# Kernel tuning notes

Hardware: AMD Instinct MI355X
Metric: run time of the kernel (lower is better)

## Reference

```python
import jax, jax.numpy as jnp
import numpy as np

B, T, C, H = 2, 2048, 1024, 16
HS = C // H                      # head_size = 64
LAYER_IDX = 2
LAMBDA_INIT = 0.8 - 0.6 * float(np.exp(-0.3 * (LAYER_IDX - 1)))
EPS = 1e-12


def setup_inputs() -> dict:
    key = jax.random.key(0)
    ks = jax.random.split(key, 22)
    std = 0.02
    w = lambda k, shape: (jax.random.normal(k, shape, jnp.float32) * std)
    inp = {
        'q': jax.random.normal(ks[0], (B, T, C), jnp.float32),
        'k': jax.random.normal(ks[1], (B, T, C), jnp.float32),
        'v': jax.random.normal(ks[2], (B, T, C), jnp.float32),
        'mask': jax.random.randint(ks[3], (B, T), 0, 2).astype(jnp.int32),
        # projection weights stored as (in, out) so y = x @ W + b
        'Wq1': w(ks[4], (C, C)), 'bq1': jnp.zeros((C,), jnp.float32),
        'Wq2': w(ks[5], (C, C)), 'bq2': jnp.zeros((C,), jnp.float32),
        'Wk1': w(ks[6], (C, C)), 'bk1': jnp.zeros((C,), jnp.float32),
        'Wk2': w(ks[7], (C, C)), 'bk2': jnp.zeros((C,), jnp.float32),
        'Wv':  w(ks[8], (C, 2 * C)), 'bv': jnp.zeros((2 * C,), jnp.float32),
        'Wc':  w(ks[9], (2 * C, C)), 'bc': jnp.zeros((C,), jnp.float32),
        'ln_w': jnp.ones((2 * HS,), jnp.float32),
        'ln_b': jnp.zeros((2 * HS,), jnp.float32),
        'lq1': jax.random.normal(ks[10], (H, HS), jnp.float32) * 0.1,
        'lk1': jax.random.normal(ks[11], (H, HS), jnp.float32) * 0.1,
        'lq2': jax.random.normal(ks[12], (H, HS), jnp.float32) * 0.1,
        'lk2': jax.random.normal(ks[13], (H, HS), jnp.float32) * 0.1,
    }
    return inp


def reference(q, k, v, mask, Wq1, bq1, Wq2, bq2, Wk1, bk1, Wk2, bk2,
              Wv, bv, Wc, bc, ln_w, ln_b, lq1, lk1, lq2, lk2):
    def heads(x, d):  # [B,T,H*d] -> [B,H,T,d]
        return x.reshape(B, T, H, d).transpose(0, 2, 1, 3)

    q1 = heads(q @ Wq1 + bq1, HS)
    q2 = heads(q @ Wq2 + bq2, HS)
    k1 = heads(k @ Wk1 + bk1, HS)
    k2 = heads(k @ Wk2 + bk2, HS)
    vv = heads(v @ Wv + bv, 2 * HS)          # [B,H,T,2*HS]

    scale = 1.0 / np.sqrt(HS)
    att1 = jnp.einsum('bhqd,bhkd->bhqk', q1, k1) * scale
    att2 = jnp.einsum('bhqd,bhkd->bhqk', q2, k2) * scale

    m = (mask == 0)[:, None, :, None]         # [B,1,Tq,1] -> masks query rows
    att1 = jnp.where(m, -1e9, att1)
    att2 = jnp.where(m, -1e9, att2)
    att1 = jax.nn.softmax(att1, axis=-1)
    att2 = jax.nn.softmax(att2, axis=-1)

    lam1 = jnp.exp(jnp.sum(lq1 * lk1, axis=-1))   # [H]
    lam2 = jnp.exp(jnp.sum(lq2 * lk2, axis=-1))
    lam = (lam1 - lam2 + LAMBDA_INIT)[None, :, None, None]
    att = att1 - lam * att2                       # differential attention

    y = jnp.einsum('bhqk,bhkd->bhqd', att, vv)    # [B,H,T,2*HS]

    # per-head TF-style LayerNorm over 2*HS, then (1 - lambda_init) scale
    u = y.mean(-1, keepdims=True)
    s = ((y - u) ** 2).mean(-1, keepdims=True)
    y = ln_w * ((y - u) / jnp.sqrt(s + EPS)) + ln_b
    y = y * (1.0 - LAMBDA_INIT)

    y = y.transpose(0, 2, 1, 3).reshape(B, T, 2 * C)
    return y @ Wc + bc
```

## Files before the change

### kernel.cpp

```cpp
#include <hip/hip_runtime.h>
#include <hip/hip_bf16.h>
#include <stdint.h>


#define T_SEQ 2048

typedef unsigned short u16;
typedef __attribute__((ext_vector_type(8))) short short8;
typedef __attribute__((ext_vector_type(4))) float f32x4;
typedef __attribute__((ext_vector_type(16))) float f32x16;

#define LAMBDA_INIT 0.35550906759096926f
#define ONE_MINUS_LI 0.6444909324090307f
#define SM_SCALE 0.125f
#define LOG2E 1.44269504f

__device__ __forceinline__ u16 f2bf(float f) {
  uint32_t u = __float_as_uint(f);
  return (u16)((u + 0x7FFFu + ((u >> 16) & 1u)) >> 16);
}
__device__ __forceinline__ float b2f(u16 u) {
  return __uint_as_float(((uint32_t)u) << 16);
}
__device__ __forceinline__ short8 ld8(const u16* p) {
  return *reinterpret_cast<const short8*>(p);
}
__device__ __forceinline__ void st8(u16* p, short8 v) {
  *reinterpret_cast<short8*>(p) = v;
}
__device__ __forceinline__ f32x4 mfma16(short8 a, short8 b, f32x4 c) {
  return __builtin_amdgcn_mfma_f32_16x16x32_bf16(a, b, c, 0, 0, 0);
}
__device__ __forceinline__ f32x16 mfma32(short8 a, short8 b, f32x16 c) {
  return __builtin_amdgcn_mfma_f32_32x32x16_bf16(a, b, c, 0, 0, 0);
}
__device__ __forceinline__ uint32_t cvtpk(float lo, float hi_) {
  uint32_t r;
  asm("v_cvt_pk_bf16_f32 %0, %1, %2" : "=v"(r) : "v"(lo), "v"(hi_));
  return r;
}

__global__ __launch_bounds__(256) void cvt_bf16(const float* __restrict__ in,
                                                u16* __restrict__ out, int n) {
  int i = (blockIdx.x * 256 + threadIdx.x) * 4;
  if (i >= n) return;
  float4 f = *reinterpret_cast<const float4*>(in + i);
  union { u16 u[4]; uint2 v; } pk;
  pk.u[0] = f2bf(f.x); pk.u[1] = f2bf(f.y); pk.u[2] = f2bf(f.z); pk.u[3] = f2bf(f.w);
  *reinterpret_cast<uint2*>(out + i) = pk.v;
}

__global__ __launch_bounds__(256) void tcvt(const float* __restrict__ W,
                                            u16* __restrict__ WT,
                                            int K, int N, int outRowOff) {
  __shared__ float tile[32][33];
  int n0 = blockIdx.x * 32, k0 = blockIdx.y * 32;
  int tx = threadIdx.x & 31, ty = threadIdx.x >> 5;
#pragma unroll
  for (int p = 0; p < 4; ++p)
    tile[ty + 8 * p][tx] = W[(size_t)(k0 + ty + 8 * p) * N + n0 + tx];
  __syncthreads();
#pragma unroll
  for (int p = 0; p < 4; ++p)
    WT[(size_t)(outRowOff + n0 + ty + 8 * p) * K + k0 + tx] = f2bf(tile[tx][ty + 8 * p]);
}

__global__ __launch_bounds__(256) void bias_concat(const float* __restrict__ b1,
                                                   const float* __restrict__ b2,
                                                   float* __restrict__ out) {
  int i = blockIdx.x * 256 + threadIdx.x;
  out[i] = (i < 1024) ? b1[i] : b2[i - 1024];
}

#define BM 128
#define BN 128
#define BK 64

template <int EPI, bool QK>
__global__ __launch_bounds__(256) void gemm_bt(const u16* __restrict__ A,
                                               const u16* __restrict__ BT,
                                               const float* __restrict__ bias,
                                               void* __restrict__ Cv,
                                               int M, int N, int K) {
  __shared__ __align__(16) u16 As[BM * BK];
  __shared__ __align__(16) u16 Bs[BN * BK];
  int t = threadIdx.x;
  int w = t >> 6, l = t & 63;
  int g = l >> 4, c16 = l & 15;
  int wr = w >> 1, wc = w & 1;
  size_t gm = (size_t)blockIdx.y * BM, gn = (size_t)blockIdx.x * BN;
  if (QK && gm >= 4096) {
    BT += (size_t)2048 * 1024;
    bias += 2048;
  }

  f32x4 acc[4][4] = {};

  int srow = l >> 3;
  int scol = (l & 7) * 8;
  const u16* Ag = A + (gm + w * 32 + srow) * (size_t)K + scol;
  const u16* Bg = BT + (gn + w * 32 + srow) * (size_t)K + scol;

  for (int kt = 0; kt < K; kt += BK) {
    __syncthreads();
#pragma unroll
    for (int c = 0; c < 4; ++c) {
      __builtin_amdgcn_global_load_lds(
          (const __attribute__((address_space(1))) void*)(Ag + (size_t)(c * 8) * K + kt),
          (__attribute__((address_space(3))) void*)&As[(w * 32 + c * 8) * BK], 16, 0, 0);
      __builtin_amdgcn_global_load_lds(
          (const __attribute__((address_space(1))) void*)(Bg + (size_t)(c * 8) * K + kt),
          (__attribute__((address_space(3))) void*)&Bs[(w * 32 + c * 8) * BK], 16, 0, 0);
    }
    __syncthreads();
#pragma unroll
    for (int kk = 0; kk < 2; ++kk) {
      short8 af[4], bf[4];
#pragma unroll
      for (int m = 0; m < 4; ++m)
        af[m] = *reinterpret_cast<const short8*>(
            &As[(wr * 64 + m * 16 + c16) * BK + kk * 32 + g * 8]);
#pragma unroll
      for (int n = 0; n < 4; ++n)
        bf[n] = *reinterpret_cast<const short8*>(
            &Bs[(wc * 64 + n * 16 + c16) * BK + kk * 32 + g * 8]);
#pragma unroll
      for (int m = 0; m < 4; ++m)
#pragma unroll
        for (int n = 0; n < 4; ++n)
          acc[m][n] = mfma16(af[m], bf[n], acc[m][n]);
    }
  }

#pragma unroll
  for (int m = 0; m < 4; ++m)
#pragma unroll
    for (int n = 0; n < 4; ++n) {
      int row0 = (int)gm + wr * 64 + m * 16 + g * 4;
      int col = (int)gn + wc * 64 + n * 16 + c16;
      float bz = bias[col];
      if (EPI == 0) {
        u16* C = (u16*)Cv;
#pragma unroll
        for (int r = 0; r < 4; ++r)
          C[(size_t)(row0 + r) * N + col] = f2bf(acc[m][n][r] + bz);
      } else if (EPI == 1) {
        u16* C = (u16*)Cv;
        int bb = row0 >> 11, tt = row0 & 2047;
        union { u16 u[4]; uint2 v; } pk;
#pragma unroll
        for (int r = 0; r < 4; ++r) pk.u[r] = f2bf(acc[m][n][r] + bz);
        *reinterpret_cast<uint2*>(&C[((size_t)(bb * 2048 + col)) * 2048 + tt]) = pk.v;
      } else {
        float* C = (float*)Cv;
#pragma unroll
        for (int r = 0; r < 4; ++r)
          C[(size_t)(row0 + r) * N + col] = acc[m][n][r] + bz;
      }
    }
}

#define KROW 72
#define YROW 72
__global__ __launch_bounds__(256, 3) void diffattn(
    const u16* __restrict__ q1q2, const u16* __restrict__ k1k2,
    const u16* __restrict__ vvT, const int* __restrict__ mask,
    const float* __restrict__ lq1, const float* __restrict__ lk1,
    const float* __restrict__ lq2, const float* __restrict__ lk2,
    const float* __restrict__ lnw, const float* __restrict__ lnb,
    u16* __restrict__ yout) {
  __shared__ __align__(16) u16 smem[18432];
  u16* Ksm = smem;
  u16* Vsm = smem + 9216;
  u16* Ysm = smem;

  int tid = threadIdx.x;
  int w = tid >> 6, l = tid & 63;
  int q = l & 31, hi = l >> 5;
  int pair = w >> 1, stream = w & 1;

  int id = blockIdx.x;
  int j = id & 7, rest = id >> 3;
  int xblk = rest & 31, ygrp = rest >> 5;
  int bh = ygrp * 8 + j;
  int b = bh >> 4, h = bh & 15;
  int qr0 = xblk * 64 + pair * 32;

  float lm1 = lq1[h * 64 + l] * lk1[h * 64 + l];
  float lm2 = lq2[h * 64 + l] * lk2[h * 64 + l];
#pragma unroll
  for (int o = 32; o; o >>= 1) {
    lm1 += __shfl_xor(lm1, o);
    lm2 += __shfl_xor(lm2, o);
  }
  float lam = __expf(lm1) - __expf(lm2) + LAMBDA_INIT;

  int soff = stream * 1024;
  const u16* qrow = q1q2 + (size_t)(b * T_SEQ + qr0 + q) * 2048 + h * 64 + soff + hi * 8;
  short8 qf[4];
#pragma unroll
  for (int c = 0; c < 4; ++c) qf[c] = ld8(qrow + c * 16);

  float scale = (mask[b * T_SEQ + qr0 + q] == 0) ? 0.f : (SM_SCALE * LOG2E);

  float M = -INFINITY, L = 0.f;
  f32x16 acc[4] = {};

  int srw = tid >> 1, shalf = tid & 1;
  int kstream = srw >> 6, kkey = srw & 63;
  const u16* srcK =
      k1k2 + (size_t)(b * T_SEQ + kkey) * 2048 + h * 64 + kstream * 1024 + shalf * 32;
  u16* dstK = &Ksm[srw * KROW + shalf * 32];
  const u16* srcV = vvT + ((size_t)(b * 16 + h) * 128 + srw) * 2048 + shalf * 32;
  u16* dstV = &Vsm[srw * KROW + shalf * 32];

  short8 kpre[4], vpre[4];
#pragma unroll
  for (int u = 0; u < 4; ++u) {
    kpre[u] = ld8(srcK + u * 8);
    vpre[u] = ld8(srcV + u * 8);
  }

  for (int kt = 0; kt < T_SEQ; kt += 64) {
    __syncthreads();
#pragma unroll
    for (int u = 0; u < 4; ++u) {
      st8(dstK + u * 8, kpre[u]);
      st8(dstV + u * 8, vpre[u]);
    }
    __syncthreads();
    if (kt + 64 < T_SEQ) {
      const u16* nk = srcK + (size_t)(kt + 64) * 2048;
      const u16* nv = srcV + (kt + 64);
#pragma unroll
      for (int u = 0; u < 4; ++u) {
        kpre[u] = ld8(nk + u * 8);
        vpre[u] = ld8(nv + u * 8);
      }
    }

#pragma unroll
    for (int st = 0; st < 2; ++st) {
      const u16* kbase = &Ksm[(stream * 64 + st * 32 + q) * KROW + hi * 8];
      short8 kf[4];
#pragma unroll
      for (int c = 0; c < 4; ++c) kf[c] = ld8(kbase + c * 16);

      f32x16 s = {};
#pragma unroll
      for (int c = 0; c < 4; ++c) s = mfma32(kf[c], qf[c], s);

      float m0 = fmaxf(fmaxf(s[0], s[1]), s[2]);
      float m1 = fmaxf(fmaxf(s[3], s[4]), s[5]);
      float m2 = fmaxf(fmaxf(s[6], s[7]), s[8]);
      float m3 = fmaxf(fmaxf(s[9], s[10]), s[11]);
      float m4 = fmaxf(fmaxf(s[12], s[13]), s[14]);
      float ma = fmaxf(fmaxf(m0, m1), m2);
      float mb = fmaxf(fmaxf(m3, m4), s[15]);
      float rm = fmaxf(ma, mb);
      rm = fmaxf(rm, __shfl_xor(rm, 32));
      float tm = rm * scale;

      if (!__all(tm - M <= 11.5f)) {
        float Mn = fmaxf(M, tm);
        float a = exp2f(M - Mn);
        L *= a;
#pragma unroll
        for (int d = 0; d < 4; ++d) acc[d] *= a;
        M = Mn;
      }

      float p[16];
#pragma unroll
      for (int r = 0; r < 16; ++r) p[r] = exp2f(__builtin_fmaf(s[r], scale, -M));
      float s8[8], s4[4];
#pragma unroll
      for (int i = 0; i < 8; ++i) s8[i] = p[i] + p[i + 8];
#pragma unroll
      for (int i = 0; i < 4; ++i) s4[i] = s8[i] + s8[i + 4];
      float ps = (s4[0] + s4[1]) + (s4[2] + s4[3]);
      ps += __shfl_xor(ps, 32);
      L += ps;

      uint32_t a1 = cvtpk(p[0], p[1]), a2 = cvtpk(p[2], p[3]);
      uint32_t b1 = cvtpk(p[4], p[5]), b2 = cvtpk(p[6], p[7]);
      uint32_t c1 = cvtpk(p[8], p[9]), c2 = cvtpk(p[10], p[11]);
      uint32_t d1 = cvtpk(p[12], p[13]), d2 = cvtpk(p[14], p[15]);
      uint32_t sa1 = (uint32_t)__shfl_xor((int)a1, 32), sa2 = (uint32_t)__shfl_xor((int)a2, 32);
      uint32_t sb1 = (uint32_t)__shfl_xor((int)b1, 32), sb2 = (uint32_t)__shfl_xor((int)b2, 32);
      uint32_t sc1 = (uint32_t)__shfl_xor((int)c1, 32), sc2 = (uint32_t)__shfl_xor((int)c2, 32);
      uint32_t sd1 = (uint32_t)__shfl_xor((int)d1, 32), sd2 = (uint32_t)__shfl_xor((int)d2, 32);
      union { uint32_t u[4]; short8 s8v; } pu0, pu1;
      pu0.u[0] = hi ? sb1 : a1;  pu0.u[1] = hi ? sb2 : a2;
      pu0.u[2] = hi ? b1 : sa1;  pu0.u[3] = hi ? b2 : sa2;
      pu1.u[0] = hi ? sd1 : c1;  pu1.u[1] = hi ? sd2 : c2;
      pu1.u[2] = hi ? d1 : sc1;  pu1.u[3] = hi ? d2 : sc2;
      short8 pf0 = pu0.s8v, pf1 = pu1.s8v;

#pragma unroll
      for (int d = 0; d < 4; ++d) {
        const u16* vb0 = &Vsm[(d * 32 + q) * KROW + st * 32 + hi * 8];
        short8 vf0 = ld8(vb0);
        short8 vf1 = ld8(vb0 + 16);
        acc[d] = mfma32(vf0, pf0, acc[d]);
        acc[d] = mfma32(vf1, pf1, acc[d]);
      }
    }
  }

  float inv = 1.f / L;
  __syncthreads();
  if (stream == 1) {
    u16* yrow = &Ysm[(pair * 64 + l) * YROW];
#pragma unroll
    for (int d = 0; d < 4; ++d) {
      union { uint32_t u[8]; short8 v[2]; } pk;
#pragma unroll
      for (int i = 0; i < 8; ++i)
        pk.u[i] = cvtpk(acc[d][2 * i] * inv, acc[d][2 * i + 1] * inv);
      st8(yrow + d * 16, pk.v[0]);
      st8(yrow + d * 16 + 8, pk.v[1]);
    }
  }
  __syncthreads();
  if (stream == 0) {
    const u16* yrow = &Ysm[(pair * 64 + l) * YROW];
    float y[4][16];
#pragma unroll
    for (int d = 0; d < 4; ++d) {
      short8 y2a = ld8(yrow + d * 16);
      short8 y2b = ld8(yrow + d * 16 + 8);
#pragma unroll
      for (int i = 0; i < 8; ++i) {
        y[d][i] = acc[d][i] * inv - lam * b2f((u16)y2a[i]);
        y[d][8 + i] = acc[d][8 + i] * inv - lam * b2f((u16)y2b[i]);
      }
    }
    float sm = 0.f;
#pragma unroll
    for (int d = 0; d < 4; ++d)
#pragma unroll
      for (int r = 0; r < 16; ++r) sm += y[d][r];
    sm += __shfl_xor(sm, 32);
    float u = sm * (1.f / 128.f);
    float var = 0.f;
#pragma unroll
    for (int d = 0; d < 4; ++d)
#pragma unroll
      for (int r = 0; r < 16; ++r) { float dd = y[d][r] - u; var += dd * dd; }
    var += __shfl_xor(var, 32);
    float rstd = rsqrtf(var * (1.f / 128.f) + 1e-12f);

    size_t orow = (size_t)(b * T_SEQ + qr0 + q) * 2048 + h * 128;
#pragma unroll
    for (int d = 0; d < 4; ++d)
#pragma unroll
      for (int rr = 0; rr < 4; ++rr) {
        int base = d * 32 + 8 * rr + 4 * hi;
        union { u16 u[4]; uint2 v; } o;
#pragma unroll
        for (int i = 0; i < 4; ++i) {
          float yv = (lnw[base + i] * ((y[d][rr * 4 + i] - u) * rstd) + lnb[base + i]) *
                     ONE_MINUS_LI;
          o.u[i] = f2bf(yv);
        }
        *reinterpret_cast<uint2*>(&yout[orow + base]) = o.v;
      }
  }
}

extern "C" void kernel_launch(void* const* d_in, const int* in_sizes, int n_in,
                              void* d_out, int out_size, void* d_ws, size_t ws_size,
                              hipStream_t stream) {
  (void)in_sizes; (void)n_in; (void)out_size; (void)ws_size;
  const float* q   = (const float*)d_in[0];
  const float* k   = (const float*)d_in[1];
  const float* v   = (const float*)d_in[2];
  const int* maskp = (const int*)d_in[3];
  const float* Wq1 = (const float*)d_in[4];
  const float* bq1 = (const float*)d_in[5];
  const float* Wq2 = (const float*)d_in[6];
  const float* bq2 = (const float*)d_in[7];
  const float* Wk1 = (const float*)d_in[8];
  const float* bk1 = (const float*)d_in[9];
  const float* Wk2 = (const float*)d_in[10];
  const float* bk2 = (const float*)d_in[11];
  const float* Wv  = (const float*)d_in[12];
  const float* bv  = (const float*)d_in[13];
  const float* Wc  = (const float*)d_in[14];
  const float* bc  = (const float*)d_in[15];
  const float* lnw = (const float*)d_in[16];
  const float* lnb = (const float*)d_in[17];
  const float* lq1 = (const float*)d_in[18];
  const float* lk1 = (const float*)d_in[19];
  const float* lq2 = (const float*)d_in[20];
  const float* lk2 = (const float*)d_in[21];

  char* ws = (char*)d_ws;
  u16* qb     = (u16*)(ws + 0);
  u16* kb     = (u16*)(ws + 8388608);
  u16* vb     = (u16*)(ws + 16777216);
  u16* Wq12T  = (u16*)(ws + 25165824);
  u16* Wk12T  = (u16*)(ws + 29360128);
  u16* WvT    = (u16*)(ws + 33554432);
  u16* WcT    = (u16*)(ws + 37748736);
  float* biasq = (float*)(ws + 41943040);
  float* biask = (float*)(ws + 41951232);
  u16* q1q2   = (u16*)(ws + 41959424);
  u16* k1k2   = (u16*)(ws + 58736640);
  u16* vvT    = (u16*)(ws + 75513856);
  u16* yb     = (u16*)(ws + 0);

  const int NELEM = 2 * T_SEQ * 1024;

  cvt_bf16<<<4096, 256, 0, stream>>>(q, qb, NELEM);
  cvt_bf16<<<4096, 256, 0, stream>>>(k, kb, NELEM);
  cvt_bf16<<<4096, 256, 0, stream>>>(v, vb, NELEM);

  tcvt<<<dim3(32, 32), 256, 0, stream>>>(Wq1, Wq12T, 1024, 1024, 0);
  tcvt<<<dim3(32, 32), 256, 0, stream>>>(Wq2, Wq12T, 1024, 1024, 1024);
  tcvt<<<dim3(32, 32), 256, 0, stream>>>(Wk1, Wk12T, 1024, 1024, 0);
  tcvt<<<dim3(32, 32), 256, 0, stream>>>(Wk2, Wk12T, 1024, 1024, 1024);
  tcvt<<<dim3(64, 32), 256, 0, stream>>>(Wv, WvT, 1024, 2048, 0);
  tcvt<<<dim3(32, 64), 256, 0, stream>>>(Wc, WcT, 2048, 1024, 0);

  bias_concat<<<8, 256, 0, stream>>>(bq1, bq2, biasq);
  bias_concat<<<8, 256, 0, stream>>>(bk1, bk2, biask);

  gemm_bt<0, true><<<dim3(16, 64), 256, 0, stream>>>(qb, Wq12T, biasq, q1q2,
                                                     8192, 2048, 1024);
  gemm_bt<1, false><<<dim3(16, 32), 256, 0, stream>>>(vb, WvT, bv, vvT, 4096, 2048, 1024);

  diffattn<<<1024, 256, 0, stream>>>(q1q2, k1k2, vvT, maskp,
                                     lq1, lk1, lq2, lk2, lnw, lnb, yb);

  gemm_bt<2, false><<<dim3(8, 32), 256, 0, stream>>>(yb, WcT, bc, d_out, 4096, 1024, 2048);
}
```

Before: 327.7 us.

## Use head-contiguous K layout and larger 512-thread attention blocks

```diff
diff --git a/kernel.cpp b/kernel.cpp
--- a/kernel.cpp
+++ b/kernel.cpp
@@ -139,31 +139,41 @@
       int row0 = (int)gm + wr * 64 + m * 16 + g * 4;
       int col = (int)gn + wc * 64 + n * 16 + c16;
       float bz = bias[col];
-      if (EPI == 0) {
-        u16* C = (u16*)Cv;
-#pragma unroll
-        for (int r = 0; r < 4; ++r)
-          C[(size_t)(row0 + r) * N + col] = f2bf(acc[m][n][r] + bz);
-      } else if (EPI == 1) {
+      if (EPI == 1) {
         u16* C = (u16*)Cv;
         int bb = row0 >> 11, tt = row0 & 2047;
         union { u16 u[4]; uint2 v; } pk;
 #pragma unroll
         for (int r = 0; r < 4; ++r) pk.u[r] = f2bf(acc[m][n][r] + bz);
         *reinterpret_cast<uint2*>(&C[((size_t)(bb * 2048 + col)) * 2048 + tt]) = pk.v;
-      } else {
+      } else if (EPI == 2) {
         float* C = (float*)Cv;
 #pragma unroll
         for (int r = 0; r < 4; ++r)
           C[(size_t)(row0 + r) * N + col] = acc[m][n][r] + bz;
+      } else {
+        u16* C = (u16*)Cv;
+        if (row0 < 4096) {
+#pragma unroll
+          for (int r = 0; r < 4; ++r)
+            C[(size_t)(row0 + r) * N + col] = f2bf(acc[m][n][r] + bz);
+        } else {
+          int t0 = row0 - 4096;
+          int bb = t0 >> 11, tt = t0 & 2047;
+          int str = col >> 10, hh = (col >> 6) & 15, dd = col & 63;
+          u16* KT = C + 8388608;
+          size_t base = (((size_t)(bb * 2 + str) * 16 + hh) * 2048 + tt) * (size_t)64 + dd;
+#pragma unroll
+          for (int r = 0; r < 4; ++r) KT[base + (size_t)r * 64] = f2bf(acc[m][n][r] + bz);
+        }
       }
     }
 }
 
 #define KROW 72
 #define YROW 72
-__global__ __launch_bounds__(256, 3) void diffattn(
-    const u16* __restrict__ q1q2, const u16* __restrict__ k1k2,
+__global__ __launch_bounds__(512, 4) void diffattn(
+    const u16* __restrict__ q1q2, const u16* __restrict__ kT,
     const u16* __restrict__ vvT, const int* __restrict__ mask,
     const float* __restrict__ lq1, const float* __restrict__ lk1,
     const float* __restrict__ lq2, const float* __restrict__ lk2,
@@ -181,10 +191,10 @@
 
   int id = blockIdx.x;
   int j = id & 7, rest = id >> 3;
-  int xblk = rest & 31, ygrp = rest >> 5;
+  int xblk = rest & 15, ygrp = rest >> 4;
   int bh = ygrp * 8 + j;
   int b = bh >> 4, h = bh & 15;
-  int qr0 = xblk * 64 + pair * 32;
+  int qr0 = xblk * 128 + pair * 32;
 
   float lm1 = lq1[h * 64 + l] * lk1[h * 64 + l];
   float lm2 = lq2[h * 64 + l] * lk2[h * 64 + l];
@@ -203,40 +213,32 @@
 
   float scale = (mask[b * T_SEQ + qr0 + q] == 0) ? 0.f : (SM_SCALE * LOG2E);
 
-  float M = -INFINITY, L = 0.f;
+  float M = -INFINITY, Lp = 0.f;
   f32x16 acc[4] = {};
 
-  int srw = tid >> 1, shalf = tid & 1;
-  int kstream = srw >> 6, kkey = srw & 63;
-  const u16* srcK =
-      k1k2 + (size_t)(b * T_SEQ + kkey) * 2048 + h * 64 + kstream * 1024 + shalf * 32;
-  u16* dstK = &Ksm[srw * KROW + shalf * 32];
-  const u16* srcV = vvT + ((size_t)(b * 16 + h) * 128 + srw) * 2048 + shalf * 32;
-  u16* dstV = &Vsm[srw * KROW + shalf * 32];
-
-  short8 kpre[4], vpre[4];
-#pragma unroll
-  for (int u = 0; u < 4; ++u) {
-    kpre[u] = ld8(srcK + u * 8);
-    vpre[u] = ld8(srcV + u * 8);
-  }
+  int skey = tid >> 3, sd = (tid & 7) * 8;
+  const u16* srcK0 = kT + (((size_t)(b * 2 + 0) * 16 + h) * 2048 + skey) * 64 + sd;
+  const u16* srcK1 = kT + (((size_t)(b * 2 + 1) * 16 + h) * 2048 + skey) * 64 + sd;
+  u16* dstK0 = &Ksm[skey * KROW + sd];
+  u16* dstK1 = &Ksm[(64 + skey) * KROW + sd];
+  int vd0 = tid >> 3, tcol = (tid & 7) * 8;
+  const u16* srcV0 = vvT + ((size_t)(b * 16 + h) * 128 + vd0) * 2048 + tcol;
+  const u16* srcV1 = vvT + ((size_t)(b * 16 + h) * 128 + 64 + vd0) * 2048 + tcol;
+  u16* dstV0 = &Vsm[vd0 * KROW + tcol];
+  u16* dstV1 = &Vsm[(64 + vd0) * KROW + tcol];
+
+  short8 kp0 = ld8(srcK0), kp1 = ld8(srcK1);
+  short8 vp0 = ld8(srcV0), vp1 = ld8(srcV1);
 
   for (int kt = 0; kt < T_SEQ; kt += 64) {
     __syncthreads();
-#pragma unroll
-    for (int u = 0; u < 4; ++u) {
-      st8(dstK + u * 8, kpre[u]);
-      st8(dstV + u * 8, vpre[u]);
-    }
+    st8(dstK0, kp0); st8(dstK1, kp1);
+    st8(dstV0, vp0); st8(dstV1, vp1);
     __syncthreads();
     if (kt + 64 < T_SEQ) {
-      const u16* nk = srcK + (size_t)(kt + 64) * 2048;
-      const u16* nv = srcV + (kt + 64);
-#pragma unroll
-      for (int u = 0; u < 4; ++u) {
-        kpre[u] = ld8(nk + u * 8);
-        vpre[u] = ld8(nv + u * 8);
-      }
+      size_t ko = (size_t)(kt + 64) * 64;
+      kp0 = ld8(srcK0 + ko); kp1 = ld8(srcK1 + ko);
+      vp0 = ld8(srcV0 + kt + 64); vp1 = ld8(srcV1 + kt + 64);
     }
 
 #pragma unroll
@@ -264,7 +266,7 @@
       if (!__all(tm - M <= 11.5f)) {
         float Mn = fmaxf(M, tm);
         float a = exp2f(M - Mn);
-        L *= a;
+        Lp *= a;
 #pragma unroll
         for (int d = 0; d < 4; ++d) acc[d] *= a;
         M = Mn;
@@ -278,9 +280,7 @@
       for (int i = 0; i < 8; ++i) s8[i] = p[i] + p[i + 8];
 #pragma unroll
       for (int i = 0; i < 4; ++i) s4[i] = s8[i] + s8[i + 4];
-      float ps = (s4[0] + s4[1]) + (s4[2] + s4[3]);
-      ps += __shfl_xor(ps, 32);
-      L += ps;
+      Lp += (s4[0] + s4[1]) + (s4[2] + s4[3]);
 
       uint32_t a1 = cvtpk(p[0], p[1]), a2 = cvtpk(p[2], p[3]);
       uint32_t b1 = cvtpk(p[4], p[5]), b2 = cvtpk(p[6], p[7]);
@@ -308,6 +308,7 @@
     }
   }
 
+  float L = Lp + __shfl_xor(Lp, 32);
   float inv = 1.f / L;
   __syncthreads();
   if (stream == 1) {
@@ -407,7 +408,7 @@
   float* biasq = (float*)(ws + 41943040);
   float* biask = (float*)(ws + 41951232);
   u16* q1q2   = (u16*)(ws + 41959424);
-  u16* k1k2   = (u16*)(ws + 58736640);
+  u16* kT     = (u16*)(ws + 58736640);
   u16* vvT    = (u16*)(ws + 75513856);
   u16* yb     = (u16*)(ws + 0);
 
@@ -427,12 +428,12 @@
   bias_concat<<<8, 256, 0, stream>>>(bq1, bq2, biasq);
   bias_concat<<<8, 256, 0, stream>>>(bk1, bk2, biask);
 
-  gemm_bt<0, true><<<dim3(16, 64), 256, 0, stream>>>(qb, Wq12T, biasq, q1q2,
+  gemm_bt<4, true><<<dim3(16, 64), 256, 0, stream>>>(qb, Wq12T, biasq, q1q2,
                                                      8192, 2048, 1024);
   gemm_bt<1, false><<<dim3(16, 32), 256, 0, stream>>>(vb, WvT, bv, vvT, 4096, 2048, 1024);
 
-  diffattn<<<1024, 256, 0, stream>>>(q1q2, k1k2, vvT, maskp,
-                                     lq1, lk1, lq2, lk2, lnw, lnb, yb);
+  diffattn<<<512, 512, 0, stream>>>(q1q2, kT, vvT, maskp,
+                                    lq1, lk1, lq2, lk2, lnw, lnb, yb);
 
   gemm_bt<2, false><<<dim3(8, 32), 256, 0, stream>>>(yb, WcT, bc, d_out, 4096, 1024, 2048);
 }
```

Result: slower. 387.7 us (+18.3%).
